# Kernel optimization log

Measured on AMD Instinct MI355X. Metric: run time of the kernel, lower is better.

## Reference

```python
import jax, jax.numpy as jnp
import numpy as np

B, S, D_IN, UNITS = 4, 4096, 256, 64


def setup_inputs() -> dict:
    key = jax.random.key(0)
    ks = jax.random.split(key, 4)
    scale = 1.0 / np.sqrt(D_IN)
    return {
        "x": jax.random.normal(ks[0], (B, S, D_IN), dtype=jnp.float32),
        "Wq": jax.random.normal(ks[1], (D_IN, UNITS), dtype=jnp.float32) * scale,
        "bq": jnp.zeros((UNITS,), dtype=jnp.float32),
        "Wk": jax.random.normal(ks[2], (D_IN, UNITS), dtype=jnp.float32) * scale,
        "bk": jnp.zeros((UNITS,), dtype=jnp.float32),
        "Wv": jax.random.normal(ks[3], (D_IN, UNITS), dtype=jnp.float32) * scale,
        "bv": jnp.zeros((UNITS,), dtype=jnp.float32),
    }


def reference(x, Wq, bq, Wk, bk, Wv, bv):
    # Q/K/V projections: [B, S, D_IN] @ [D_IN, UNITS] -> [B, S, UNITS]
    q = jnp.einsum("bsd,du->bsu", x, Wq) + bq
    k = jnp.einsum("bsd,du->bsu", x, Wk) + bk
    v = jnp.einsum("bsd,du->bsu", x, Wv) + bv
    # Full [B, S, S] scores (the module materializes these - headroom target)
    sims = jnp.einsum("bsu,btu->bst", q, k) / np.sqrt(UNITS).astype(np.float32)
    attn = jax.nn.softmax(sims, axis=-1)
    out = jnp.einsum("bst,btu->bsu", attn, v)
    return out  # activation is None (linear)
```

## Files before the change

### kernel.cpp

```cpp
#include <hip/hip_runtime.h>
#include <hip/hip_bf16.h>

#define B_ 4
#define S_ 4096
#define D_ 256
#define U_ 64
#define NROWS (B_ * S_)
#define QSCALE 0.1803368801111244f

typedef __attribute__((ext_vector_type(8))) short short8;
typedef __attribute__((ext_vector_type(8))) float float8;
typedef __attribute__((ext_vector_type(4))) float floatx4;

__device__ inline short f2bf(float f) {
    union { __hip_bfloat16 h; short s; } u;
    u.h = __float2bfloat16(f);
    return u.s;
}
__device__ inline unsigned pk2bf(float a, float b) {
    unsigned ua = __float_as_uint(a) + 0x8000u;
    unsigned ub = __float_as_uint(b) + 0x8000u;
    return (ub & 0xFFFF0000u) | (ua >> 16);
}
__device__ inline float fast_exp2(float x) {
#if __has_builtin(__builtin_amdgcn_exp2f)
    return __builtin_amdgcn_exp2f(x);
#else
    return exp2f(x);
#endif
}

__global__ void pack_w_kernel(const float* __restrict__ Wq,
                              const float* __restrict__ Wk,
                              const float* __restrict__ Wv,
                              short* __restrict__ wpack) {
    int tid = blockIdx.x * 256 + threadIdx.x;
    if (tid >= 3 * 16384) return;
    int p = tid >> 14, e = tid & 16383;
    const float* W = (p == 0) ? Wq : (p == 1) ? Wk : Wv;
    float w = W[e];
    int k = e >> 6, n = e & 63;
    int ks = k >> 5, hi = (k >> 3) & 3, j = k & 7;
    int l = hi * 16 + (n & 15), nc = n >> 4;
    wpack[p * 16384 + ((ks * 4 + nc) * 64 + l) * 8 + j] = f2bf(w);
}

__global__ __launch_bounds__(256) void qkv_proj_kernel(
    const float* __restrict__ x, const short* __restrict__ wpack,
    const float* __restrict__ bq, const float* __restrict__ bk,
    const float* __restrict__ bv,
    short* __restrict__ Q, short* __restrict__ Kpack, short* __restrict__ Vpack) {
    __shared__ __align__(16) short k_sh[64][72];
    __shared__ __align__(16) short vT_sh[64][72];
    const int wl    = threadIdx.x >> 6;
    const int lane  = threadIdx.x & 63;
    const int col16 = lane & 15, quad = lane >> 4;
    const int m0b = blockIdx.x * 64, m0 = m0b + wl * 16;

    floatx4 acc[3][4];
#pragma unroll
    for (int p = 0; p < 3; ++p)
#pragma unroll
        for (int nc = 0; nc < 4; ++nc) acc[p][nc] = (floatx4){0.f, 0.f, 0.f, 0.f};

    const float* xrow = x + (size_t)(m0 + col16) * D_ + quad * 8;
#pragma unroll
    for (int ks = 0; ks < 8; ++ks) {
        float8 af = *(const float8*)(xrow + ks * 32);
        short8 a;
#pragma unroll
        for (int j = 0; j < 8; ++j) a[j] = f2bf(af[j]);
#pragma unroll
        for (int p = 0; p < 3; ++p) {
#pragma unroll
            for (int nc = 0; nc < 4; ++nc) {
                short8 bfr = *(const short8*)(wpack +
                    ((size_t)((p * 8 + ks) * 4 + nc) * 64 + lane) * 8);
                acc[p][nc] = __builtin_amdgcn_mfma_f32_16x16x32_bf16(a, bfr, acc[p][nc], 0, 0, 0);
            }
        }
    }

#pragma unroll
    for (int nc = 0; nc < 4; ++nc) {
        float biasq = bq[nc * 16 + col16];
        float biask = bk[nc * 16 + col16];
        float biasv = bv[nc * 16 + col16];
#pragma unroll
        for (int r = 0; r < 4; ++r) {
            int row = m0 + quad * 4 + r;
            Q[(size_t)row * U_ + nc * 16 + col16] = f2bf((acc[0][nc][r] + biasq) * QSCALE);
            k_sh[wl * 16 + quad * 4 + r][nc * 16 + col16] = f2bf(acc[1][nc][r] + biask);
        }
        union { short s[4]; unsigned long long u; } pv;
#pragma unroll
        for (int r = 0; r < 4; ++r) pv.s[r] = f2bf(acc[2][nc][r] + biasv);
        *(unsigned long long*)&vT_sh[nc * 16 + col16][wl * 16 + quad * 4] = pv.u;
    }
    __syncthreads();

#pragma unroll
    for (int c2 = 0; c2 < 2; ++c2) {
        int combo = wl + c2 * 4;
        int ww = combo >> 2, t = (combo >> 1) & 1, h = combo & 1;
        int srow = ww * 32 + (col16 >> 2) * 8 + (col16 & 3) + 4 * t;
        short8 v = *(const short8*)&k_sh[srow][h * 32 + quad * 8];
        size_t gt = (size_t)blockIdx.x * 2 + ww;
        *(short8*)(Kpack + (gt * 4 + t * 2 + h) * 512 + lane * 8) = v;
    }
#pragma unroll
    for (int c2 = 0; c2 < 2; ++c2) {
        int combo = wl + c2 * 4;
        int ww = combo >> 2, nc = combo & 3;
        short8 v = *(const short8*)&vT_sh[nc * 16 + col16][ww * 32 + quad * 8];
        size_t gt = (size_t)blockIdx.x * 2 + ww;
        *(short8*)(Vpack + (gt * 4 + nc) * 512 + lane * 8) = v;
    }
}

__global__ __launch_bounds__(256) void attn_kernel(
    const short* __restrict__ Q, const short* __restrict__ Kpack,
    const short* __restrict__ Vpack, float* __restrict__ oslab,
    float* __restrict__ lslab) {
    __shared__ __align__(16) short lds[2][4096];

    const int i  = blockIdx.x;
    const int b  = (i & 7) >> 1;
    const int r  = ((i >> 3) << 1) | (i & 1);
    const int kw = r & 3, qb = r >> 2;
    const int w  = threadIdx.x >> 6;
    const int lane  = threadIdx.x & 63;
    const int col16 = lane & 15, quad = lane >> 4;
    const int q0 = qb * 64 + w * 16;

    const short* qrow = Q + ((size_t)(b * S_ + q0 + col16)) * U_ + quad * 8;
    short8 bQ0 = *(const short8*)(qrow);
    short8 bQ1 = *(const short8*)(qrow + 32);

    floatx4 o[4];
#pragma unroll
    for (int nc = 0; nc < 4; ++nc) o[nc] = (floatx4){0.f, 0.f, 0.f, 0.f};
    float l_i = 0.f;

    const int tb = b * 128 + kw * 32;
    const short* kg = Kpack + (size_t)tb * 2048 + w * 512 + lane * 8;
    const short* vg = Vpack + (size_t)tb * 2048 + w * 512 + lane * 8;

    short8 gk = *(const short8*)(kg);
    short8 gv = *(const short8*)(vg);
    *(short8*)&lds[0][w * 512 + lane * 8]        = gk;
    *(short8*)&lds[0][2048 + w * 512 + lane * 8] = gv;
    __syncthreads();

    for (int it = 0; it < 32; ++it) {
        const int cur = it & 1;
        if (it + 1 < 32) {
            gk = *(const short8*)(kg + (size_t)(it + 1) * 2048);
            gv = *(const short8*)(vg + (size_t)(it + 1) * 2048);
        }
        const short* base = lds[cur];
        short8 ak[2][2];
#pragma unroll
        for (int t = 0; t < 2; ++t)
#pragma unroll
            for (int h = 0; h < 2; ++h)
                ak[t][h] = *(const short8*)(base + (t * 2 + h) * 512 + lane * 8);
        short8 av[4];
#pragma unroll
        for (int nc = 0; nc < 4; ++nc)
            av[nc] = *(const short8*)(base + 2048 + nc * 512 + lane * 8);

        floatx4 c[2];
#pragma unroll
        for (int t = 0; t < 2; ++t) {
            c[t] = __builtin_amdgcn_mfma_f32_16x16x32_bf16(ak[t][0], bQ0,
                      (floatx4){0.f, 0.f, 0.f, 0.f}, 0, 0, 0);
            c[t] = __builtin_amdgcn_mfma_f32_16x16x32_bf16(ak[t][1], bQ1, c[t], 0, 0, 0);
        }
        float p[8];
        float rs = 0.f;
#pragma unroll
        for (int t = 0; t < 2; ++t)
#pragma unroll
            for (int rr = 0; rr < 4; ++rr) {
                float e = fast_exp2(c[t][rr]);
                p[t * 4 + rr] = e;
                rs += e;
            }
        l_i += rs;
        union { short8 s; unsigned u[4]; } pb;
        pb.u[0] = pk2bf(p[0], p[1]);
        pb.u[1] = pk2bf(p[2], p[3]);
        pb.u[2] = pk2bf(p[4], p[5]);
        pb.u[3] = pk2bf(p[6], p[7]);
#pragma unroll
        for (int nc = 0; nc < 4; ++nc)
            o[nc] = __builtin_amdgcn_mfma_f32_16x16x32_bf16(av[nc], pb.s, o[nc], 0, 0, 0);

        if (it + 1 < 32) {
            *(short8*)&lds[cur ^ 1][w * 512 + lane * 8]        = gk;
            *(short8*)&lds[cur ^ 1][2048 + w * 512 + lane * 8] = gv;
        }
        __syncthreads();
    }

    l_i += __shfl_xor(l_i, 16, 64);
    l_i += __shfl_xor(l_i, 32, 64);
    if (quad == 0)
        lslab[(size_t)kw * NROWS + b * S_ + q0 + col16] = l_i;

    float* fl = (float*)lds + w * 1024;
#pragma unroll
    for (int nc = 0; nc < 4; ++nc)
#pragma unroll
        for (int rr = 0; rr < 4; ++rr)
            fl[col16 * 64 + nc * 16 + quad * 4 + rr] = o[nc][rr];
    asm volatile("s_waitcnt lgkmcnt(0)" ::: "memory");
    float* dst = oslab + ((size_t)kw * NROWS + b * S_ + q0) * U_ + lane * 16;
#pragma unroll
    for (int v4 = 0; v4 < 4; ++v4)
        *(float4*)(dst + v4 * 4) = *(float4*)(fl + lane * 16 + v4 * 4);
}

__global__ __launch_bounds__(256) void merge_kernel(
    const float* __restrict__ oslab, const float* __restrict__ lslab,
    float* __restrict__ out) {
    int idx = blockIdx.x * 256 + threadIdx.x;
    int row = idx >> 6;
    float s = oslab[idx] + oslab[idx + (size_t)NROWS * 64]
            + oslab[idx + (size_t)2 * NROWS * 64] + oslab[idx + (size_t)3 * NROWS * 64];
    float l = lslab[row] + lslab[row + NROWS]
            + lslab[row + 2 * NROWS] + lslab[row + 3 * NROWS];
    out[idx] = s / l;
}

extern "C" void kernel_launch(void* const* d_in, const int* in_sizes, int n_in,
                              void* d_out, int out_size, void* d_ws, size_t ws_size,
                              hipStream_t stream) {
    const float* x  = (const float*)d_in[0];
    const float* Wq = (const float*)d_in[1];
    const float* bq = (const float*)d_in[2];
    const float* Wk = (const float*)d_in[3];
    const float* bk = (const float*)d_in[4];
    const float* Wv = (const float*)d_in[5];
    const float* bv = (const float*)d_in[6];
    float* out = (float*)d_out;

    short* Q     = (short*)d_ws;
    short* Kpack = Q + (size_t)NROWS * U_;
    short* Vpack = Kpack + (size_t)NROWS * U_;
    short* wpack = Vpack + (size_t)NROWS * U_;
    float* oslab = (float*)(wpack + 65536);
    float* lslab = oslab + (size_t)4 * NROWS * 64;

    pack_w_kernel<<<192, 256, 0, stream>>>(Wq, Wk, Wv, wpack);
    qkv_proj_kernel<<<NROWS / 64, 256, 0, stream>>>(
        x, wpack, bq, bk, bv, Q, Kpack, Vpack);
    attn_kernel<<<1024, 256, 0, stream>>>(Q, Kpack, Vpack, oslab, lslab);
    merge_kernel<<<NROWS * 64 / 256, 256, 0, stream>>>(oslab, lslab, out);
}
```

Before: 121.4 us.

## Drop LDS staging in attention, split keys eight ways, write fragment-order slabs

The attention kernel now reads packed K/V fragments straight from global memory instead of double-buffering them through LDS, uses 512-thread blocks covering 128 queries, and splits the key range into eight chunks instead of four. Partial outputs are stored directly in MFMA fragment order, which removes the LDS transpose at the end. The merge kernel now sums eight slabs and undoes the fragment permutation when writing the output. This removes LDS traffic and per-iteration barriers but relies on L1/L2 to serve repeated K/V reads, and it doubles the partial-slab traffic the merge kernel has to read. A barrier on every other iteration remains, apparently to keep the waves in step.

Result: slower. 139.0 us (+14.4%).

```diff
diff --git a/kernel.cpp b/kernel.cpp
--- a/kernel.cpp
+++ b/kernel.cpp
@@ -118,22 +118,20 @@
     }
 }
 
-__global__ __launch_bounds__(256) void attn_kernel(
+__global__ __launch_bounds__(512) void attn_kernel(
     const short* __restrict__ Q, const short* __restrict__ Kpack,
     const short* __restrict__ Vpack, float* __restrict__ oslab,
     float* __restrict__ lslab) {
-    __shared__ __align__(16) short lds[2][4096];
-
     const int i  = blockIdx.x;
     const int b  = (i & 7) >> 1;
     const int r  = ((i >> 3) << 1) | (i & 1);
-    const int kw = r & 3, qb = r >> 2;
+    const int kw = r & 7, qb = r >> 3;
     const int w  = threadIdx.x >> 6;
     const int lane  = threadIdx.x & 63;
     const int col16 = lane & 15, quad = lane >> 4;
-    const int q0 = qb * 64 + w * 16;
-
-    const short* qrow = Q + ((size_t)(b * S_ + q0 + col16)) * U_ + quad * 8;
+    const int q0 = qb * 128 + w * 16;
+
+    const short* qrow = Q + (size_t)(b * S_ + q0 + col16) * U_ + quad * 8;
     short8 bQ0 = *(const short8*)(qrow);
     short8 bQ1 = *(const short8*)(qrow + 32);
 
@@ -142,33 +140,22 @@
     for (int nc = 0; nc < 4; ++nc) o[nc] = (floatx4){0.f, 0.f, 0.f, 0.f};
     float l_i = 0.f;
 
-    const int tb = b * 128 + kw * 32;
-    const short* kg = Kpack + (size_t)tb * 2048 + w * 512 + lane * 8;
-    const short* vg = Vpack + (size_t)tb * 2048 + w * 512 + lane * 8;
-
-    short8 gk = *(const short8*)(kg);
-    short8 gv = *(const short8*)(vg);
-    *(short8*)&lds[0][w * 512 + lane * 8]        = gk;
-    *(short8*)&lds[0][2048 + w * 512 + lane * 8] = gv;
-    __syncthreads();
-
-    for (int it = 0; it < 32; ++it) {
-        const int cur = it & 1;
-        if (it + 1 < 32) {
-            gk = *(const short8*)(kg + (size_t)(it + 1) * 2048);
-            gv = *(const short8*)(vg + (size_t)(it + 1) * 2048);
-        }
-        const short* base = lds[cur];
+    const short* kbase = Kpack + ((size_t)(b * 128 + kw * 16)) * 2048 + lane * 8;
+    const short* vbase = Vpack + ((size_t)(b * 128 + kw * 16)) * 2048 + lane * 8;
+
+    for (int it = 0; it < 16; ++it) {
+        const short* kp = kbase + it * 2048;
+        const short* vp = vbase + it * 2048;
         short8 ak[2][2];
 #pragma unroll
         for (int t = 0; t < 2; ++t)
 #pragma unroll
             for (int h = 0; h < 2; ++h)
-                ak[t][h] = *(const short8*)(base + (t * 2 + h) * 512 + lane * 8);
+                ak[t][h] = *(const short8*)(kp + (t * 2 + h) * 512);
         short8 av[4];
 #pragma unroll
         for (int nc = 0; nc < 4; ++nc)
-            av[nc] = *(const short8*)(base + 2048 + nc * 512 + lane * 8);
+            av[nc] = *(const short8*)(vp + nc * 512);
 
         floatx4 c[2];
 #pragma unroll
@@ -197,11 +184,7 @@
         for (int nc = 0; nc < 4; ++nc)
             o[nc] = __builtin_amdgcn_mfma_f32_16x16x32_bf16(av[nc], pb.s, o[nc], 0, 0, 0);
 
-        if (it + 1 < 32) {
-            *(short8*)&lds[cur ^ 1][w * 512 + lane * 8]        = gk;
-            *(short8*)&lds[cur ^ 1][2048 + w * 512 + lane * 8] = gv;
-        }
-        __syncthreads();
+        if (it & 1) __syncthreads();
     }
 
     l_i += __shfl_xor(l_i, 16, 64);
@@ -209,29 +192,29 @@
     if (quad == 0)
         lslab[(size_t)kw * NROWS + b * S_ + q0 + col16] = l_i;
 
-    float* fl = (float*)lds + w * 1024;
+    const int tg = (b * S_ + q0) >> 4;
+    float* dst = oslab + (((size_t)kw * 1024 + tg) * 64 + lane) * 16;
 #pragma unroll
     for (int nc = 0; nc < 4; ++nc)
-#pragma unroll
-        for (int rr = 0; rr < 4; ++rr)
-            fl[col16 * 64 + nc * 16 + quad * 4 + rr] = o[nc][rr];
-    asm volatile("s_waitcnt lgkmcnt(0)" ::: "memory");
-    float* dst = oslab + ((size_t)kw * NROWS + b * S_ + q0) * U_ + lane * 16;
-#pragma unroll
-    for (int v4 = 0; v4 < 4; ++v4)
-        *(float4*)(dst + v4 * 4) = *(float4*)(fl + lane * 16 + v4 * 4);
+        *(float4*)(dst + nc * 4) = *(const float4*)&o[nc];
 }
 
 __global__ __launch_bounds__(256) void merge_kernel(
     const float* __restrict__ oslab, const float* __restrict__ lslab,
     float* __restrict__ out) {
     int idx = blockIdx.x * 256 + threadIdx.x;
-    int row = idx >> 6;
-    float s = oslab[idx] + oslab[idx + (size_t)NROWS * 64]
-            + oslab[idx + (size_t)2 * NROWS * 64] + oslab[idx + (size_t)3 * NROWS * 64];
-    float l = lslab[row] + lslab[row + NROWS]
-            + lslab[row + 2 * NROWS] + lslab[row + 3 * NROWS];
-    out[idx] = s / l;
+    float s = 0.f;
+#pragma unroll
+    for (int kw = 0; kw < 8; ++kw)
+        s += oslab[(size_t)kw * (1024 * 64 * 16) + idx];
+    int tg = idx >> 10, lane = (idx >> 4) & 63, reg = idx & 15;
+    int row = tg * 16 + (lane & 15);
+    int col = (reg >> 2) * 16 + (lane >> 4) * 4 + (reg & 3);
+    float lt = 0.f;
+#pragma unroll
+    for (int kw = 0; kw < 8; ++kw)
+        lt += lslab[(size_t)kw * NROWS + row];
+    out[(size_t)row * U_ + col] = s / lt;
 }
 
 extern "C" void kernel_launch(void* const* d_in, const int* in_sizes, int n_in,
@@ -251,11 +234,11 @@
     short* Vpack = Kpack + (size_t)NROWS * U_;
     short* wpack = Vpack + (size_t)NROWS * U_;
     float* oslab = (float*)(wpack + 65536);
-    float* lslab = oslab + (size_t)4 * NROWS * 64;
+    float* lslab = oslab + (size_t)8 * 1024 * 64 * 16;
 
     pack_w_kernel<<<192, 256, 0, stream>>>(Wq, Wk, Wv, wpack);
     qkv_proj_kernel<<<NROWS / 64, 256, 0, stream>>>(
         x, wpack, bq, bk, bv, Q, Kpack, Vpack);
-    attn_kernel<<<1024, 256, 0, stream>>>(Q, Kpack, Vpack, oslab, lslab);
-    merge_kernel<<<NROWS * 64 / 256, 256, 0, stream>>>(oslab, lslab, out);
-}
+    attn_kernel<<<1024, 512, 0, stream>>>(Q, Kpack, Vpack, oslab, lslab);
+    merge_kernel<<<1024 * 64 * 16 / 256, 256, 0, stream>>>(oslab, lslab, out);
+}
```
